# Kernel tuning notes

Measured on AMD Instinct MI355X. Metric: run time of the kernel, lower is better.

Reference implementation:

```python
import jax, jax.numpy as jnp
import numpy as np

N_NODES = 50000
N_EDGES = 800000
D_IN = 256
D_HID = 256
D_OUT = 256


def sage_conv(x, src, dst, W_l, b_l, W_r, num_nodes):
    """PyG SAGEConv with mean aggregation: lin_l(mean_{j in N(i)} x_j) + lin_r(x_i)."""
    msg = x[src]  # [E, C] gather of source-node features
    agg = jax.ops.segment_sum(msg, dst, num_segments=num_nodes)  # [N, C]
    cnt = jax.ops.segment_sum(jnp.ones((src.shape[0],), x.dtype), dst,
                              num_segments=num_nodes)
    mean = agg / jnp.maximum(cnt, 1.0)[:, None]  # isolated nodes -> 0
    return mean @ W_l.T + b_l + x @ W_r.T


def setup_inputs() -> dict:
    key = jax.random.key(0)
    ks = jax.random.split(key, 10)
    s = 1.0 / np.sqrt(D_IN)
    x = jax.random.normal(ks[0], (N_NODES, D_IN), dtype=jnp.float32)
    edge_index = jax.random.randint(ks[1], (2, N_EDGES), 0, N_NODES, dtype=jnp.int64)
    mention_index = jax.random.randint(ks[2], (1,), 0, N_NODES, dtype=jnp.int64)
    return {
        "x": x,
        "edge_index": edge_index,
        "mention_index": mention_index,
        "W1_l": jax.random.uniform(ks[3], (D_HID, D_IN), jnp.float32, -s, s),
        "b1_l": jnp.zeros((D_HID,), jnp.float32),
        "W1_r": jax.random.uniform(ks[4], (D_HID, D_IN), jnp.float32, -s, s),
        "W2_l": jax.random.uniform(ks[5], (D_OUT, D_HID), jnp.float32, -s, s),
        "b2_l": jnp.zeros((D_OUT,), jnp.float32),
        "W2_r": jax.random.uniform(ks[6], (D_OUT, D_HID), jnp.float32, -s, s),
    }


def reference(x, edge_index, mention_index, W1_l, b1_l, W1_r, W2_l, b2_l, W2_r):
    src, dst = edge_index[0], edge_index[1]
    h = jax.nn.relu(sage_conv(x, src, dst, W1_l, b1_l, W1_r, N_NODES))
    h = sage_conv(h, src, dst, W2_l, b2_l, W2_r, N_NODES)
    # dropout in the original is a no-op (result discarded)
    logits = (h[mention_index] * h).sum(axis=1)  # [N]
    z = jax.nn.softmax(logits, axis=0)
    return z
```

## Files before the change

kernel.cpp:

```cpp
#include <hip/hip_runtime.h>
#include <math.h>

#define N_NODES 50000
#define N_EDGES 800000
#define D 256
#define K2 512
#define M_PAD 50048
#define BM 128
#define BN 128
#define BK 32
#define SCAN_B 196
#define SM_B 49

typedef __attribute__((ext_vector_type(8))) short short8;
typedef __attribute__((ext_vector_type(8))) unsigned short ushort8;
typedef __attribute__((ext_vector_type(4))) float floatx4;

__device__ __forceinline__ unsigned short bf16_rn(float f) {
    union { float f; unsigned u; } a; a.f = f;
    unsigned r = a.u + 0x7FFF + ((a.u >> 16) & 1);
    return (unsigned short)(r >> 16);
}
__device__ __forceinline__ float bf16_to_f(unsigned short h) {
    union { unsigned u; float f; } a; a.u = ((unsigned)h) << 16;
    return a.f;
}
__device__ __forceinline__ void load_lds16(const void* g, void* lds) {
    __builtin_amdgcn_global_load_lds((const __attribute__((address_space(1))) void*)g,
                                     (__attribute__((address_space(3))) void*)lds, 16, 0, 0);
}

__global__ void k_count(const int* __restrict__ dst, int* __restrict__ deg) {
    int e = blockIdx.x * blockDim.x + threadIdx.x;
    if (e < N_EDGES) atomicAdd(&deg[dst[e]], 1);
}

__global__ void k_scan1(const int* __restrict__ deg, int* __restrict__ bsum) {
    __shared__ int red[256];
    int b = blockIdx.x, t = threadIdx.x;
    int i = b * 256 + t;
    red[t] = (i < N_NODES) ? deg[i] : 0;
    __syncthreads();
    for (int o = 128; o; o >>= 1) {
        if (t < o) red[t] += red[t + o];
        __syncthreads();
    }
    if (t == 0) bsum[b] = red[0];
}

__global__ void k_scan2(const int* __restrict__ bsum, int* __restrict__ boff) {
    __shared__ int sh[256];
    int t = threadIdx.x;
    sh[t] = (t < SCAN_B) ? bsum[t] : 0;
    __syncthreads();
    for (int o = 1; o < 256; o <<= 1) {
        int v = (t >= o) ? sh[t - o] : 0;
        __syncthreads();
        sh[t] += v;
        __syncthreads();
    }
    boff[t] = (t == 0) ? 0 : sh[t - 1];
}

__global__ void k_scan3(const int* __restrict__ deg, const int* __restrict__ boff,
                        int* __restrict__ cursor) {
    __shared__ int sh[256];
    int b = blockIdx.x, t = threadIdx.x;
    int i = b * 256 + t;
    int v = (i < N_NODES) ? deg[i] : 0;
    sh[t] = v;
    __syncthreads();
    for (int o = 1; o < 256; o <<= 1) {
        int val = (t >= o) ? sh[t - o] : 0;
        __syncthreads();
        sh[t] += val;
        __syncthreads();
    }
    if (i < N_NODES) cursor[i] = boff[b] + sh[t] - v;
}

__global__ void k_bucket(const int* __restrict__ src, const int* __restrict__ dst,
                         int* __restrict__ cursor, int* __restrict__ csr_src) {
    int e = blockIdx.x * blockDim.x + threadIdx.x;
    if (e >= N_EDGES) return;
    int pos = atomicAdd(&cursor[dst[e]], 1);
    csr_src[pos] = src[e];
}

__global__ void k_splitX(const float* __restrict__ x, unsigned short* __restrict__ Ahi,
                         unsigned short* __restrict__ Alo) {
    int t = blockIdx.x * blockDim.x + threadIdx.x;
    if (t >= N_NODES * 64) return;
    int m = t >> 6, j = (t & 63) * 4;
    float4 v = *(const float4*)&x[(size_t)m * D + j];
    ushort4 hi, lo;
    hi.x = bf16_rn(v.x); lo.x = bf16_rn(v.x - bf16_to_f(hi.x));
    hi.y = bf16_rn(v.y); lo.y = bf16_rn(v.y - bf16_to_f(hi.y));
    hi.z = bf16_rn(v.z); lo.z = bf16_rn(v.z - bf16_to_f(hi.z));
    hi.w = bf16_rn(v.w); lo.w = bf16_rn(v.w - bf16_to_f(hi.w));
    *(ushort4*)&Ahi[(size_t)m * K2 + 256 + j] = hi;
    *(ushort4*)&Alo[(size_t)m * K2 + 256 + j] = lo;
}

__global__ void k_splitB(const float* __restrict__ Wl, const float* __restrict__ Wr,
                         unsigned short* __restrict__ Bhi, unsigned short* __restrict__ Blo) {
    int t = blockIdx.x * blockDim.x + threadIdx.x;
    if (t >= 256 * 128) return;
    int n = t >> 7, k = (t & 127) * 4;
    const float* srcp = (k < 256) ? &Wl[(size_t)n * 256 + k] : &Wr[(size_t)n * 256 + k - 256];
    float4 v = *(const float4*)srcp;
    ushort4 hi, lo;
    hi.x = bf16_rn(v.x); lo.x = bf16_rn(v.x - bf16_to_f(hi.x));
    hi.y = bf16_rn(v.y); lo.y = bf16_rn(v.y - bf16_to_f(hi.y));
    hi.z = bf16_rn(v.z); lo.z = bf16_rn(v.z - bf16_to_f(hi.z));
    hi.w = bf16_rn(v.w); lo.w = bf16_rn(v.w - bf16_to_f(hi.w));
    *(ushort4*)&Bhi[(size_t)n * K2 + k] = hi;
    *(ushort4*)&Blo[(size_t)n * K2 + k] = lo;
}

__global__ __launch_bounds__(256) void k_agg(const int* __restrict__ cursor,
                                             const int* __restrict__ deg,
                                             const int* __restrict__ csr,
                                             unsigned short* __restrict__ Ahi,
                                             unsigned short* __restrict__ Alo) {
    int node = blockIdx.x * 4 + (threadIdx.x >> 6);
    int lane = threadIdx.x & 63;
    if (node >= N_NODES) return;
    int d = deg[node], end = cursor[node], start = end - d;
    int h = lane >> 5;
    int col = (lane & 31) * 8;
    float acc0[8] = {}, acc1[8] = {};
    int j = start;
    for (; j + 4 <= end; j += 4) {
        int i0 = csr[j + h];
        int i1 = csr[j + 2 + h];
        ushort8 v0 = *(const ushort8*)&Ahi[(size_t)i0 * K2 + 256 + col];
        ushort8 v1 = *(const ushort8*)&Ahi[(size_t)i1 * K2 + 256 + col];
        #pragma unroll
        for (int k = 0; k < 8; k++) {
            acc0[k] += bf16_to_f(v0[k]);
            acc1[k] += bf16_to_f(v1[k]);
        }
    }
    if (j + 2 <= end) {
        int i0 = csr[j + h];
        ushort8 v0 = *(const ushort8*)&Ahi[(size_t)i0 * K2 + 256 + col];
        #pragma unroll
        for (int k = 0; k < 8; k++) acc0[k] += bf16_to_f(v0[k]);
        j += 2;
    }
    if (j < end && h == 0) {
        int i0 = csr[j];
        ushort8 v0 = *(const ushort8*)&Ahi[(size_t)i0 * K2 + 256 + col];
        #pragma unroll
        for (int k = 0; k < 8; k++) acc0[k] += bf16_to_f(v0[k]);
    }
    float inv = 1.0f / fmaxf((float)d, 1.0f);
    ushort8 hi, lo;
    #pragma unroll
    for (int k = 0; k < 8; k++) {
        float a = acc0[k] + acc1[k];
        a += __shfl_xor(a, 32);
        float m = a * inv;
        hi[k] = bf16_rn(m);
        lo[k] = bf16_rn(m - bf16_to_f(hi[k]));
    }
    if (h == 0) {
        *(ushort8*)&Ahi[(size_t)node * K2 + col] = hi;
        *(ushort8*)&Alo[(size_t)node * K2 + col] = lo;
    }
}

__global__ __launch_bounds__(256) void k_small(const int* __restrict__ mention,
                                               const int* __restrict__ deg,
                                               const int* __restrict__ cursor,
                                               const int* __restrict__ csr,
                                               const float* __restrict__ x,
                                               const float* __restrict__ W1l,
                                               const float* __restrict__ W1r,
                                               const float* __restrict__ b1,
                                               float* __restrict__ h1m) {
    int m = mention[0];
    int dm = min(deg[m], 255);
    int slot = blockIdx.x;
    if (slot > dm) return;
    int startm = cursor[m] - deg[m];
    int node = (slot == 0) ? m : csr[startm + slot - 1];
    __shared__ float smean[D], sx[D];
    int t = threadIdx.x;
    int d = deg[node], end = cursor[node], start = end - d;
    float a = 0.f;
    for (int j = start; j < end; j++) a += x[(size_t)csr[j] * D + t];
    smean[t] = a / fmaxf((float)d, 1.0f);
    sx[t] = x[(size_t)node * D + t];
    __syncthreads();
    float z = b1[t];
    for (int k = 0; k < D; k++)
        z += smean[k] * W1l[(size_t)t * D + k] + sx[k] * W1r[(size_t)t * D + k];
    h1m[(size_t)slot * D + t] = fmaxf(z, 0.f);
}

__global__ __launch_bounds__(256) void k_vu(const int* __restrict__ mention,
                                            const int* __restrict__ deg,
                                            const float* __restrict__ h1m,
                                            const float* __restrict__ W2l,
                                            const float* __restrict__ W2r,
                                            const float* __restrict__ b2,
                                            float* __restrict__ u,
                                            float* __restrict__ cout) {
    __shared__ float sm[D], sh[D], sv[D], red[256];
    int m = mention[0];
    int dm = min(deg[m], 255);
    int t = threadIdx.x;
    float a = 0.f;
    for (int j = 1; j <= dm; j++) a += h1m[(size_t)j * D + t];
    sm[t] = a / fmaxf((float)deg[m], 1.0f);
    sh[t] = h1m[t];
    __syncthreads();
    float acc = b2[t];
    for (int k = 0; k < D; k++)
        acc += sm[k] * W2l[(size_t)t * D + k] + sh[k] * W2r[(size_t)t * D + k];
    sv[t] = acc;
    red[t] = b2[t] * acc;
    __syncthreads();
    for (int o = 128; o; o >>= 1) {
        if (t < o) red[t] += red[t + o];
        __syncthreads();
    }
    if (t == 0) cout[0] = red[0];
    float a1 = 0.f, a2 = 0.f;
    for (int n = 0; n < D; n++) {
        a1 += W2l[(size_t)n * D + t] * sv[n];
        a2 += W2r[(size_t)n * D + t] * sv[n];
    }
    u[t] = a1;
    u[D + t] = a2;
}

__global__ __launch_bounds__(256, 2)
void k_gemm_fused(const unsigned short* __restrict__ Ahi,
                  const unsigned short* __restrict__ Alo,
                  const unsigned short* __restrict__ Bhi,
                  const unsigned short* __restrict__ Blo,
                  const float* __restrict__ bias,
                  const float* __restrict__ u,
                  float* __restrict__ s,
                  float* __restrict__ t_) {
    __shared__ unsigned short sA[2][BM * BK];
    __shared__ unsigned short sB[2][BN * BK];
    __shared__ float sred[BM], tred[BM];
    int tid = threadIdx.x;
    int br = blockIdx.x, bc = blockIdx.y;
    int lane = tid & 63, wv = tid >> 6;
    int wm = (wv >> 1) * 64, wn = (wv & 1) * 64;
    int q = lane >> 4, r = lane & 15;

    float biasv[4], u1v[4], u2v[4];
    #pragma unroll
    for (int nt = 0; nt < 4; nt++) {
        int gc = bc * BN + wn + nt * 16 + r;
        biasv[nt] = bias[gc];
        u1v[nt] = u[gc];
        u2v[nt] = u[256 + gc];
    }
    if (tid < BM) { sred[tid] = 0.f; tred[tid] = 0.f; }

    floatx4 acc[4][4] = {};

    const size_t arow0 = (size_t)br * BM;
    const int brow0 = bc * BN;
    int seg = lane & 3;
    int rl16 = lane >> 2;

    for (int kt = 0; kt < K2 / BK; kt++) {
        #pragma unroll
        for (int t = 0; t < 2; t++) {
            int rloc = wv * 32 + t * 16 + rl16;
            size_t gA = (arow0 + rloc) * (size_t)K2 + kt * BK + seg * 8;
            size_t gB = (size_t)(brow0 + rloc) * K2 + kt * BK + seg * 8;
            int ldsoff = (wv * 32 + t * 16) * BK;
            load_lds16(Ahi + gA, &sA[0][ldsoff]);
            load_lds16(Alo + gA, &sA[1][ldsoff]);
            load_lds16(Bhi + gB, &sB[0][ldsoff]);
            load_lds16(Blo + gB, &sB[1][ldsoff]);
        }
        __syncthreads();
        short8 ah[4], al[4], bh[4], bl[4];
        #pragma unroll
        for (int i = 0; i < 4; i++) {
            ah[i] = *(const short8*)&sA[0][(wm + i * 16 + r) * BK + q * 8];
            al[i] = *(const short8*)&sA[1][(wm + i * 16 + r) * BK + q * 8];
            bh[i] = *(const short8*)&sB[0][(wn + i * 16 + r) * BK + q * 8];
            bl[i] = *(const short8*)&sB[1][(wn + i * 16 + r) * BK + q * 8];
        }
        #pragma unroll
        for (int mt = 0; mt < 4; mt++)
            #pragma unroll
            for (int nt = 0; nt < 4; nt++) {
                acc[mt][nt] = __builtin_amdgcn_mfma_f32_16x16x32_bf16(ah[mt], bh[nt], acc[mt][nt], 0, 0, 0);
                acc[mt][nt] = __builtin_amdgcn_mfma_f32_16x16x32_bf16(ah[mt], bl[nt], acc[mt][nt], 0, 0, 0);
                acc[mt][nt] = __builtin_amdgcn_mfma_f32_16x16x32_bf16(al[mt], bh[nt], acc[mt][nt], 0, 0, 0);
            }
        __syncthreads();
    }

    #pragma unroll
    for (int mt = 0; mt < 4; mt++) {
        #pragma unroll
        for (int reg = 0; reg < 4; reg++) {
            float sacc = 0.f, tacc = 0.f;
            #pragma unroll
            for (int nt = 0; nt < 4; nt++) {
                float h = fmaxf(acc[mt][nt][reg] + biasv[nt], 0.f);
                sacc += h * u1v[nt];
                tacc += h * u2v[nt];
            }
            #pragma unroll
            for (int off = 1; off < 16; off <<= 1) {
                sacc += __shfl_xor(sacc, off);
                tacc += __shfl_xor(tacc, off);
            }
            if (r == 0) {
                int row = wm + mt * 16 + q * 4 + reg;
                atomicAdd(&sred[row], sacc);
                atomicAdd(&tred[row], tacc);
            }
        }
    }
    __syncthreads();
    if (tid < BM) {
        size_t grow = arow0 + tid;
        if (grow < N_NODES) {
            atomicAdd(&s[grow], sred[tid]);
            atomicAdd(&t_[grow], tred[tid]);
        }
    }
}

__global__ void k_logits(const int* __restrict__ deg, const int* __restrict__ cursor,
                         const int* __restrict__ csr,
                         const float* __restrict__ s, const float* __restrict__ t_,
                         const float* __restrict__ cptr, float* __restrict__ logits) {
    int i = blockIdx.x * blockDim.x + threadIdx.x;
    if (i >= N_NODES) return;
    int d = deg[i];
    int end = cursor[i];
    int start = end - d;
    float sum = 0.f;
    for (int j = start; j < end; j++) sum += s[csr[j]];
    logits[i] = sum / fmaxf((float)d, 1.0f) + t_[i] + cptr[0];
}

__global__ __launch_bounds__(1024) void k_sm1(const float* __restrict__ logits,
                                              float* __restrict__ pmax,
                                              float* __restrict__ psum) {
    __shared__ float red[1024];
    int b = blockIdx.x, t = threadIdx.x;
    int i = b * 1024 + t;
    float x = (i < N_NODES) ? logits[i] : -INFINITY;
    red[t] = x;
    __syncthreads();
    for (int o = 512; o; o >>= 1) {
        if (t < o) red[t] = fmaxf(red[t], red[t + o]);
        __syncthreads();
    }
    float mb = red[0];
    __syncthreads();
    red[t] = (i < N_NODES) ? __expf(x - mb) : 0.f;
    __syncthreads();
    for (int o = 512; o; o >>= 1) {
        if (t < o) red[t] += red[t + o];
        __syncthreads();
    }
    if (t == 0) { pmax[b] = mb; psum[b] = red[0]; }
}

__global__ void k_sm2(const float* __restrict__ pmax, const float* __restrict__ psum,
                      float* __restrict__ gS) {
    __shared__ float rm[64], rs[64];
    int t = threadIdx.x;
    float m = (t < SM_B) ? pmax[t] : -INFINITY;
    rm[t] = m;
    __syncthreads();
    for (int o = 32; o; o >>= 1) {
        if (t < o) rm[t] = fmaxf(rm[t], rm[t + o]);
        __syncthreads();
    }
    float g = rm[0];
    __syncthreads();
    rs[t] = (t < SM_B) ? psum[t] * __expf(m - g) : 0.f;
    __syncthreads();
    for (int o = 32; o; o >>= 1) {
        if (t < o) rs[t] += rs[t + o];
        __syncthreads();
    }
    if (t == 0) { gS[0] = g; gS[1] = 1.0f / rs[0]; }
}

__global__ void k_sm3(const float* __restrict__ logits, const float* __restrict__ gS,
                      float* __restrict__ out) {
    int i = blockIdx.x * blockDim.x + threadIdx.x;
    if (i < N_NODES) out[i] = __expf(logits[i] - gS[0]) * gS[1];
}

extern "C" void kernel_launch(void* const* d_in, const int* in_sizes, int n_in,
                              void* d_out, int out_size, void* d_ws, size_t ws_size,
                              hipStream_t stream) {
    const float* x   = (const float*)d_in[0];
    const int*   ei  = (const int*)d_in[1];
    const int*   src = ei;
    const int*   dst = ei + N_EDGES;
    const int*   mention = (const int*)d_in[2];
    const float* W1l = (const float*)d_in[3];
    const float* b1  = (const float*)d_in[4];
    const float* W1r = (const float*)d_in[5];
    const float* W2l = (const float*)d_in[6];
    const float* b2  = (const float*)d_in[7];
    const float* W2r = (const float*)d_in[8];

    char* w = (char*)d_ws;
    unsigned short* Ahi = (unsigned short*)w;  w += (size_t)M_PAD * K2 * 2;
    unsigned short* Alo = (unsigned short*)w;  w += (size_t)M_PAD * K2 * 2;
    unsigned short* Bhi = (unsigned short*)w;  w += (size_t)256 * K2 * 2;
    unsigned short* Blo = (unsigned short*)w;  w += (size_t)256 * K2 * 2;
    float* s     = (float*)w;  w += (size_t)N_NODES * 4;
    float* t_    = (float*)w;  w += (size_t)N_NODES * 4;
    int* deg     = (int*)w;    w += (size_t)N_NODES * 4;
    float* logit = (float*)w;  w += (size_t)N_NODES * 4;
    float* h1m   = (float*)w;  w += (size_t)256 * D * 4;
    float* u     = (float*)w;  w += 2 * D * 4;
    float* c     = (float*)w;  w += 16;
    float* pmax  = (float*)w;  w += 64 * 4;
    float* psum  = (float*)w;  w += 64 * 4;
    float* gS    = (float*)w;  w += 16;
    int* cursor  = (int*)w;    w += (size_t)N_NODES * 4;
    int* bsum    = (int*)w;    w += 256 * 4;
    int* boff    = (int*)w;    w += 256 * 4;
    int* csr     = (int*)w;    w += (size_t)N_EDGES * 4;

    hipMemsetAsync(s, 0, (size_t)3 * N_NODES * sizeof(float), stream);

    k_count <<<(N_EDGES + 255) / 256, 256, 0, stream>>>(dst, deg);
    k_scan1 <<<SCAN_B, 256, 0, stream>>>(deg, bsum);
    k_scan2 <<<1, 256, 0, stream>>>(bsum, boff);
    k_scan3 <<<SCAN_B, 256, 0, stream>>>(deg, boff, cursor);
    k_bucket<<<(N_EDGES + 255) / 256, 256, 0, stream>>>(src, dst, cursor, csr);

    k_splitX<<<(N_NODES * 64 + 255) / 256, 256, 0, stream>>>(x, Ahi, Alo);
    k_splitB<<<(256 * 128 + 255) / 256, 256, 0, stream>>>(W1l, W1r, Bhi, Blo);
    k_agg   <<<(N_NODES + 3) / 4, 256, 0, stream>>>(cursor, deg, csr, Ahi, Alo);

    k_small <<<256, 256, 0, stream>>>(mention, deg, cursor, csr, x, W1l, W1r, b1, h1m);
    k_vu    <<<1, 256, 0, stream>>>(mention, deg, h1m, W2l, W2r, b2, u, c);

    dim3 g1(M_PAD / BM, 2);
    k_gemm_fused<<<g1, 256, 0, stream>>>(Ahi, Alo, Bhi, Blo, b1, u, s, t_);

    k_logits<<<(N_NODES + 255) / 256, 256, 0, stream>>>(deg, cursor, csr, s, t_, c, logit);
    k_sm1   <<<SM_B, 1024, 0, stream>>>(logit, pmax, psum);
    k_sm2   <<<1, 64, 0, stream>>>(pmax, psum, gS);
    k_sm3   <<<(N_NODES + 255) / 256, 256, 0, stream>>>(logit, gS, (float*)d_out);
}
```

Baseline: 389.0 us.

## Widen GEMM tile to full N, drop atomics and fuse logits with softmax pass

The fused GEMM now covers all 256 output columns per block with 512 threads (8 waves). Each A row tile is loaded once instead of twice, and the per-row s/t reductions complete inside one block, so plain stores replace global atomics and the memset of s/t is no longer needed. The logits gather is fused into the first softmax reduction kernel, with 196 blocks of 256, and k_sm2 is widened to match. The larger block raises LDS and register pressure and halves the GEMM grid, which may lower occupancy.

Result: no change. 381.8 us (-1.8%).

```diff
diff --git a/kernel.cpp b/kernel.cpp
--- a/kernel.cpp
+++ b/kernel.cpp
@@ -7,10 +7,9 @@
 #define K2 512
 #define M_PAD 50048
 #define BM 128
-#define BN 128
+#define BN 256
 #define BK 32
 #define SCAN_B 196
-#define SM_B 49
 
 typedef __attribute__((ext_vector_type(8))) short short8;
 typedef __attribute__((ext_vector_type(8))) unsigned short ushort8;
@@ -237,7 +236,7 @@
     u[D + t] = a2;
 }
 
-__global__ __launch_bounds__(256, 2)
+__global__ __launch_bounds__(512, 4)
 void k_gemm_fused(const unsigned short* __restrict__ Ahi,
                   const unsigned short* __restrict__ Alo,
                   const unsigned short* __restrict__ Bhi,
@@ -250,15 +249,15 @@
     __shared__ unsigned short sB[2][BN * BK];
     __shared__ float sred[BM], tred[BM];
     int tid = threadIdx.x;
-    int br = blockIdx.x, bc = blockIdx.y;
+    int br = blockIdx.x;
     int lane = tid & 63, wv = tid >> 6;
-    int wm = (wv >> 1) * 64, wn = (wv & 1) * 64;
+    int wm = (wv >> 2) * 64, wn = (wv & 3) * 64;
     int q = lane >> 4, r = lane & 15;
 
     float biasv[4], u1v[4], u2v[4];
     #pragma unroll
     for (int nt = 0; nt < 4; nt++) {
-        int gc = bc * BN + wn + nt * 16 + r;
+        int gc = wn + nt * 16 + r;
         biasv[nt] = bias[gc];
         u1v[nt] = u[gc];
         u2v[nt] = u[256 + gc];
@@ -268,19 +267,22 @@
     floatx4 acc[4][4] = {};
 
     const size_t arow0 = (size_t)br * BM;
-    const int brow0 = bc * BN;
     int seg = lane & 3;
     int rl16 = lane >> 2;
 
     for (int kt = 0; kt < K2 / BK; kt++) {
+        {
+            int rloc = wv * 16 + rl16;
+            size_t gA = (arow0 + rloc) * (size_t)K2 + kt * BK + seg * 8;
+            int ldsoff = (wv * 16) * BK;
+            load_lds16(Ahi + gA, &sA[0][ldsoff]);
+            load_lds16(Alo + gA, &sA[1][ldsoff]);
+        }
         #pragma unroll
         for (int t = 0; t < 2; t++) {
             int rloc = wv * 32 + t * 16 + rl16;
-            size_t gA = (arow0 + rloc) * (size_t)K2 + kt * BK + seg * 8;
-            size_t gB = (size_t)(brow0 + rloc) * K2 + kt * BK + seg * 8;
+            size_t gB = (size_t)rloc * K2 + kt * BK + seg * 8;
             int ldsoff = (wv * 32 + t * 16) * BK;
-            load_lds16(Ahi + gA, &sA[0][ldsoff]);
-            load_lds16(Alo + gA, &sA[1][ldsoff]);
             load_lds16(Bhi + gB, &sB[0][ldsoff]);
             load_lds16(Blo + gB, &sB[1][ldsoff]);
         }
@@ -331,44 +333,45 @@
     if (tid < BM) {
         size_t grow = arow0 + tid;
         if (grow < N_NODES) {
-            atomicAdd(&s[grow], sred[tid]);
-            atomicAdd(&t_[grow], tred[tid]);
-        }
-    }
-}
-
-__global__ void k_logits(const int* __restrict__ deg, const int* __restrict__ cursor,
-                         const int* __restrict__ csr,
-                         const float* __restrict__ s, const float* __restrict__ t_,
-                         const float* __restrict__ cptr, float* __restrict__ logits) {
-    int i = blockIdx.x * blockDim.x + threadIdx.x;
-    if (i >= N_NODES) return;
-    int d = deg[i];
-    int end = cursor[i];
-    int start = end - d;
-    float sum = 0.f;
-    for (int j = start; j < end; j++) sum += s[csr[j]];
-    logits[i] = sum / fmaxf((float)d, 1.0f) + t_[i] + cptr[0];
-}
-
-__global__ __launch_bounds__(1024) void k_sm1(const float* __restrict__ logits,
-                                              float* __restrict__ pmax,
-                                              float* __restrict__ psum) {
-    __shared__ float red[1024];
+            s[grow] = sred[tid];
+            t_[grow] = tred[tid];
+        }
+    }
+}
+
+__global__ __launch_bounds__(256) void k_logits_sm1(const int* __restrict__ deg,
+                                                    const int* __restrict__ cursor,
+                                                    const int* __restrict__ csr,
+                                                    const float* __restrict__ s,
+                                                    const float* __restrict__ t_,
+                                                    const float* __restrict__ cptr,
+                                                    float* __restrict__ logits,
+                                                    float* __restrict__ pmax,
+                                                    float* __restrict__ psum) {
+    __shared__ float red[256];
     int b = blockIdx.x, t = threadIdx.x;
-    int i = b * 1024 + t;
-    float x = (i < N_NODES) ? logits[i] : -INFINITY;
-    red[t] = x;
-    __syncthreads();
-    for (int o = 512; o; o >>= 1) {
+    int i = b * 256 + t;
+    float lg = -INFINITY;
+    if (i < N_NODES) {
+        int d = deg[i];
+        int end = cursor[i];
+        int start = end - d;
+        float sum = 0.f;
+        for (int j = start; j < end; j++) sum += s[csr[j]];
+        lg = sum / fmaxf((float)d, 1.0f) + t_[i] + cptr[0];
+        logits[i] = lg;
+    }
+    red[t] = lg;
+    __syncthreads();
+    for (int o = 128; o; o >>= 1) {
         if (t < o) red[t] = fmaxf(red[t], red[t + o]);
         __syncthreads();
     }
     float mb = red[0];
     __syncthreads();
-    red[t] = (i < N_NODES) ? __expf(x - mb) : 0.f;
-    __syncthreads();
-    for (int o = 512; o; o >>= 1) {
+    red[t] = (i < N_NODES) ? __expf(lg - mb) : 0.f;
+    __syncthreads();
+    for (int o = 128; o; o >>= 1) {
         if (t < o) red[t] += red[t + o];
         __syncthreads();
     }
@@ -377,20 +380,20 @@
 
 __global__ void k_sm2(const float* __restrict__ pmax, const float* __restrict__ psum,
                       float* __restrict__ gS) {
-    __shared__ float rm[64], rs[64];
+    __shared__ float rm[256], rs[256];
     int t = threadIdx.x;
-    float m = (t < SM_B) ? pmax[t] : -INFINITY;
+    float m = (t < SCAN_B) ? pmax[t] : -INFINITY;
     rm[t] = m;
     __syncthreads();
-    for (int o = 32; o; o >>= 1) {
+    for (int o = 128; o; o >>= 1) {
         if (t < o) rm[t] = fmaxf(rm[t], rm[t + o]);
         __syncthreads();
     }
     float g = rm[0];
     __syncthreads();
-    rs[t] = (t < SM_B) ? psum[t] * __expf(m - g) : 0.f;
-    __syncthreads();
-    for (int o = 32; o; o >>= 1) {
+    rs[t] = (t < SCAN_B) ? psum[t] * __expf(m - g) : 0.f;
+    __syncthreads();
+    for (int o = 128; o; o >>= 1) {
         if (t < o) rs[t] += rs[t + o];
         __syncthreads();
     }
@@ -430,15 +433,15 @@
     float* h1m   = (float*)w;  w += (size_t)256 * D * 4;
     float* u     = (float*)w;  w += 2 * D * 4;
     float* c     = (float*)w;  w += 16;
-    float* pmax  = (float*)w;  w += 64 * 4;
-    float* psum  = (float*)w;  w += 64 * 4;
+    float* pmax  = (float*)w;  w += 256 * 4;
+    float* psum  = (float*)w;  w += 256 * 4;
     float* gS    = (float*)w;  w += 16;
     int* cursor  = (int*)w;    w += (size_t)N_NODES * 4;
     int* bsum    = (int*)w;    w += 256 * 4;
     int* boff    = (int*)w;    w += 256 * 4;
     int* csr     = (int*)w;    w += (size_t)N_EDGES * 4;
 
-    hipMemsetAsync(s, 0, (size_t)3 * N_NODES * sizeof(float), stream);
+    hipMemsetAsync(deg, 0, (size_t)N_NODES * sizeof(int), stream);
 
     k_count <<<(N_EDGES + 255) / 256, 256, 0, stream>>>(dst, deg);
     k_scan1 <<<SCAN_B, 256, 0, stream>>>(deg, bsum);
@@ -453,11 +456,9 @@
     k_small <<<256, 256, 0, stream>>>(mention, deg, cursor, csr, x, W1l, W1r, b1, h1m);
     k_vu    <<<1, 256, 0, stream>>>(mention, deg, h1m, W2l, W2r, b2, u, c);
 
-    dim3 g1(M_PAD / BM, 2);
-    k_gemm_fused<<<g1, 256, 0, stream>>>(Ahi, Alo, Bhi, Blo, b1, u, s, t_);
-
-    k_logits<<<(N_NODES + 255) / 256, 256, 0, stream>>>(deg, cursor, csr, s, t_, c, logit);
-    k_sm1   <<<SM_B, 1024, 0, stream>>>(logit, pmax, psum);
-    k_sm2   <<<1, 64, 0, stream>>>(pmax, psum, gS);
+    k_gemm_fused<<<M_PAD / BM, 512, 0, stream>>>(Ahi, Alo, Bhi, Blo, b1, u, s, t_);
+
+    k_logits_sm1<<<SCAN_B, 256, 0, stream>>>(deg, cursor, csr, s, t_, c, logit, pmax, psum);
+    k_sm2   <<<1, 256, 0, stream>>>(pmax, psum, gS);
     k_sm3   <<<(N_NODES + 255) / 256, 256, 0, stream>>>(logit, gS, (float*)d_out);
 }
```
